# Optimization experiments

Hardware: AMD Instinct MI355X
Metric: run time of the kernel (lower is better)

## Reference

```python
import jax, jax.numpy as jnp
import numpy as np

NF = 64      # feature channels
DG = 8       # deformable groups
KH = 3       # kernel size
K = KH * KH  # kernel points
B, H, W = 2, 256, 256


def conv2d(x, w, b):
    # 3x3, stride 1, pad 1, NCHW
    y = jax.lax.conv_general_dilated(x, w, (1, 1), [(1, 1), (1, 1)],
                                     dimension_numbers=('NCHW', 'OIHW', 'NCHW'))
    return y + b[None, :, None, None]


def bilinear_gather(img, py, px):
    # img: [B,G,Cg,H,W]; py,px: [B,G,Kd,H,W] float pixel coords (zero padding outside)
    # returns [B,G,Cg,Kd,H,W]
    b, g, cg, h, w = img.shape
    kd = py.shape[2]
    y0 = jnp.floor(py)
    x0 = jnp.floor(px)
    wy = py - y0
    wx = px - x0
    imgf = img.reshape(b, g, cg, h * w)

    def tap(yi, xi, wt):
        valid = (yi >= 0) & (yi <= h - 1) & (xi >= 0) & (xi <= w - 1)
        idx = (jnp.clip(yi, 0, h - 1) * w + jnp.clip(xi, 0, w - 1)).astype(jnp.int32)
        idxf = idx.reshape(b, g, 1, kd * h * w)
        v = jnp.take_along_axis(imgf, jnp.broadcast_to(idxf, (b, g, cg, kd * h * w)), axis=-1)
        v = v.reshape(b, g, cg, kd, h, w)
        return v * (wt * valid)[:, :, None]

    return (tap(y0, x0, (1 - wy) * (1 - wx)) + tap(y0, x0 + 1, (1 - wy) * wx)
            + tap(y0 + 1, x0, wy * (1 - wx)) + tap(y0 + 1, x0 + 1, wy * wx))


def setup_inputs() -> dict:
    key = jax.random.key(0)
    ks = jax.random.split(key, 8)
    s = 0.05
    return {
        'nbr': jax.random.normal(ks[0], (B, NF, H, W), jnp.float32),
        'ref': jax.random.normal(ks[1], (B, NF, H, W), jnp.float32),
        'optical_flow': jax.random.normal(ks[2], (B, 2, H, W), jnp.float32),
        'conv1_w': jax.random.normal(ks[3], (NF, 2 * NF, KH, KH), jnp.float32) * s,
        'conv1_b': jnp.zeros((NF,), jnp.float32),
        'om_w': jax.random.normal(ks[4], (DG * 3 * K, NF + 2, KH, KH), jnp.float32) * s,
        'om_b': jnp.zeros((DG * 3 * K,), jnp.float32),
        'dcn_w': jax.random.normal(ks[5], (NF, NF, KH, KH), jnp.float32) * s,
        'dcn_b': jnp.zeros((NF,), jnp.float32),
    }


def reference(nbr, ref, optical_flow, conv1_w, conv1_b, om_w, om_b, dcn_w, dcn_b):
    b, c, h, w = nbr.shape
    dt = nbr.dtype
    gy, gx = jnp.meshgrid(jnp.arange(h, dtype=dt), jnp.arange(w, dtype=dt), indexing='ij')

    # ---- backwarp(nbr, flow): bilinear sample at (x+fx, y+fy), zero padding ----
    py = (gy[None] + optical_flow[:, 1])[:, None, None]  # [B,1,1,H,W]
    px = (gx[None] + optical_flow[:, 0])[:, None, None]
    nbr_warp = bilinear_gather(nbr[:, None], py, px).reshape(b, c, h, w)

    # ---- offset feature ----
    fea = jax.nn.relu(conv2d(jnp.concatenate([nbr_warp, ref], 1), conv1_w, conv1_b))

    # ---- FlowGuidedDCN offset/mask generation ----
    out = conv2d(jnp.concatenate([fea, optical_flow], 1), om_w, om_b)
    o1, o2, mask = jnp.split(out, 3, axis=1)
    offset = jnp.concatenate([o1, o2], 1)                       # [B, 2*DG*K, H, W]
    flow_rep = jnp.tile(optical_flow[:, ::-1], (1, offset.shape[1] // 2, 1, 1))
    offset = offset + flow_rep
    mask = jax.nn.sigmoid(mask)                                 # [B, DG*K, H, W]

    # ---- deformable conv v2 (stride 1, pad 1, dil 1) ----
    off = offset.reshape(b, DG, K, 2, h, w)
    dy, dx = off[:, :, :, 0], off[:, :, :, 1]                   # [B,DG,K,H,W]
    ky, kx = jnp.meshgrid(jnp.arange(KH, dtype=dt), jnp.arange(KH, dtype=dt), indexing='ij')
    base_y = gy[None] - 1 + ky.reshape(-1)[:, None, None]       # [K,H,W]
    base_x = gx[None] - 1 + kx.reshape(-1)[:, None, None]
    spy = base_y[None, None] + dy
    spx = base_x[None, None] + dx

    cg = c // DG
    sampled = bilinear_gather(nbr.reshape(b, DG, cg, h, w), spy, spx)  # [B,DG,Cg,K,H,W]
    m = mask.reshape(b, DG, 1, K, h, w)
    wr = dcn_w.reshape(dcn_w.shape[0], DG, cg, K)
    y = jnp.einsum('bgckhw,ogck->bohw', sampled * m, wr) + dcn_b[None, :, None, None]
    return y
```

## Files before the change

### kernel.cpp

```cpp
#include <hip/hip_runtime.h>
#include <math.h>

#define HW 65536
#define WD 256
#define HT 256

typedef short short8 __attribute__((ext_vector_type(8)));
typedef float f32x4 __attribute__((ext_vector_type(4)));
typedef __bf16 bf16x8 __attribute__((ext_vector_type(8)));

__device__ __forceinline__ short f2bf(float f) {
    union { float f; unsigned u; } v; v.f = f;
    unsigned r = (v.u + 0x7fffu + ((v.u >> 16) & 1u)) >> 16;
    return (short)r;
}

__device__ __forceinline__ float bf2f(short s) {
    union { unsigned u; float f; } v;
    v.u = ((unsigned)(unsigned short)s) << 16;
    return v.f;
}

__device__ __forceinline__ int iclamp(int v, int lo, int hi) {
    return v < lo ? lo : (v > hi ? hi : v);
}

struct Taps {
    int i00, i01, i10, i11;
    float w00, w01, w10, w11;
};

__device__ __forceinline__ Taps make_taps(float py, float px) {
    float fy0 = floorf(py), fx0 = floorf(px);
    float wy = py - fy0, wx = px - fx0;
    int y0 = (int)fy0, x0 = (int)fx0;
    int y1 = y0 + 1, x1 = x0 + 1;
    float vy0 = (y0 >= 0 && y0 <= HT - 1) ? 1.f : 0.f;
    float vy1 = (y1 >= 0 && y1 <= HT - 1) ? 1.f : 0.f;
    float vx0 = (x0 >= 0 && x0 <= WD - 1) ? 1.f : 0.f;
    float vx1 = (x1 >= 0 && x1 <= WD - 1) ? 1.f : 0.f;
    int yc0 = iclamp(y0, 0, HT - 1), yc1 = iclamp(y1, 0, HT - 1);
    int xc0 = iclamp(x0, 0, WD - 1), xc1 = iclamp(x1, 0, WD - 1);
    Taps t;
    t.i00 = yc0 * WD + xc0; t.i01 = yc0 * WD + xc1;
    t.i10 = yc1 * WD + xc0; t.i11 = yc1 * WD + xc1;
    t.w00 = (1.f - wy) * (1.f - wx) * vy0 * vx0;
    t.w01 = (1.f - wy) * wx * vy0 * vx1;
    t.w10 = wy * (1.f - wx) * vy1 * vx0;
    t.w11 = wy * wx * vy1 * vx1;
    return t;
}

__global__ __launch_bounds__(256) void pack_x1_kernel(
    const float* __restrict__ nbr, const float* __restrict__ ref,
    const float* __restrict__ flow, short* __restrict__ X1)
{
    __shared__ short tile[64 * 130];
    int blk = blockIdx.x;
    int b = blk >> 10;
    int grp = blk & 1023;
    int px = threadIdx.x & 63;
    int qq = threadIdx.x >> 6;
    int pos = grp * 64 + px;
    int yy = pos >> 8, xx = pos & 255;

    float fx = flow[b * 2 * HW + pos];
    float fy = flow[b * 2 * HW + HW + pos];
    Taps tp = make_taps((float)yy + fy, (float)xx + fx);

    const float* nb = nbr + (size_t)b * 64 * HW;
    const float* rf = ref + (size_t)b * 64 * HW;
    #pragma unroll
    for (int j = 0; j < 16; ++j) {
        int c = qq * 16 + j;
        const float* pc = nb + c * HW;
        float v = tp.w00 * pc[tp.i00] + tp.w01 * pc[tp.i01] +
                  tp.w10 * pc[tp.i10] + tp.w11 * pc[tp.i11];
        tile[px * 130 + c] = f2bf(v);
        tile[px * 130 + 64 + c] = f2bf(rf[c * HW + pos]);
    }
    __syncthreads();

    short* xo = X1 + ((size_t)b * HW + grp * 64) * 128;
    #pragma unroll
    for (int f8 = threadIdx.x; f8 < 1024; f8 += 256) {
        int p = (f8 * 8) >> 7;
        int c = (f8 * 8) & 127;
        short8 v;
        #pragma unroll
        for (int j = 0; j < 8; ++j) v[j] = tile[p * 130 + c + j];
        *(short8*)(xo + f8 * 8) = v;
    }
}

__global__ __launch_bounds__(256) void pack_nbr_kernel(
    const float* __restrict__ nbr, short* __restrict__ N2)
{
    __shared__ short tile[64 * 66];
    int blk = blockIdx.x;
    int b = blk >> 10;
    int grp = blk & 1023;
    int px = threadIdx.x & 63;
    int qq = threadIdx.x >> 6;
    int pos = grp * 64 + px;

    const float* nb = nbr + (size_t)b * 64 * HW;
    #pragma unroll
    for (int j = 0; j < 16; ++j) {
        int c = qq * 16 + j;
        tile[px * 66 + c] = f2bf(nb[c * HW + pos]);
    }
    __syncthreads();

    short* xo = N2 + (size_t)b * HW * 64;
    #pragma unroll
    for (int f8 = threadIdx.x; f8 < 512; f8 += 256) {
        int g = f8 >> 6;
        int p = f8 & 63;
        short8 v;
        #pragma unroll
        for (int j = 0; j < 8; ++j) v[j] = tile[p * 66 + g * 8 + j];
        *(short8*)(xo + ((size_t)g * HW + grp * 64 + p) * 8) = v;
    }
}

__global__ __launch_bounds__(256) void repack_w1_kernel(
    const float* __restrict__ w, short* __restrict__ wr)
{
    int t = blockIdx.x * 256 + threadIdx.x;
    int j = t & 7, q = (t >> 3) & 3, l = (t >> 5) & 15;
    int nt = (t >> 9) & 3, kc = t >> 11;
    int k = kc * 32 + q * 8 + j;
    int rs = k >> 7, c = k & 127;
    int n = nt * 16 + l;
    wr[t] = f2bf(w[(n * 128 + c) * 9 + rs]);
}

__global__ __launch_bounds__(256) void repack_w2_kernel(
    const float* __restrict__ w, short* __restrict__ wr)
{
    int t = blockIdx.x * 256 + threadIdx.x;
    if (t >= 155648) return;
    int j = t & 7, q = (t >> 3) & 3, l = (t >> 5) & 15;
    int nt = (t >> 9) & 15, kc = t >> 13;
    int n = nt * 16 + l;
    float v = 0.f;
    if (kc < 18) {
        int k = kc * 32 + q * 8 + j;
        int rs = k >> 6, c = k & 63;
        if (n < 216) v = w[(n * 66 + c) * 9 + rs];
    } else {
        int k18 = q * 8 + j;
        if (k18 < 18 && n < 216) {
            int tap = k18 >> 1, u = k18 & 1;
            v = w[(n * 66 + 64 + u) * 9 + tap];
        }
    }
    wr[t] = f2bf(v);
}

__global__ __launch_bounds__(256) void repack_dcn_kernel(
    const float* __restrict__ w, short* __restrict__ wr)
{
    int t = blockIdx.x * 256 + threadIdx.x;
    int j = t & 7, q = (t >> 3) & 3, l = (t >> 5) & 15;
    int rem = t >> 9;
    int nt = rem & 3;
    int gkc = rem >> 2;
    int kc = gkc % 3, g = gkc / 3;
    int Kidx = kc * 32 + q * 8 + j;
    int k = Kidx >> 3, c = Kidx & 7;
    int och = nt * 16 + l;
    float v = (k < 9) ? w[(och * 64 + g * 8 + c) * 9 + k] : 0.f;
    wr[t] = f2bf(v);
}

#define PADC1 128
__global__ __launch_bounds__(256) void conv1_mfma_kernel(
    const short* __restrict__ X1, const float* __restrict__ bias,
    const short* __restrict__ wr, short* __restrict__ X2)
{
    __shared__ short lds[198 * PADC1];
    const int tid = threadIdx.x;
    const int w = __builtin_amdgcn_readfirstlane(tid >> 6);
    const int l15 = tid & 15;
    const int q = (tid >> 4) & 3;
    const int blk = ((blockIdx.x & 7) << 8) | (blockIdx.x >> 3);
    const int xseg = blk & 3;
    const int yy = (blk >> 2) & 255;
    const int b = blk >> 10;
    const int x0 = xseg * 64;

    const short* xin = X1 + (size_t)b * HW * 128;
    for (int i = tid; i < 198 * 16; i += 256) {
        int c16 = i & 15;
        int pix = i >> 4;
        int r = pix / 66, xx = pix % 66;
        int gy = yy + r - 1, gx = x0 + xx - 1;
        short8 v = {0, 0, 0, 0, 0, 0, 0, 0};
        if (gy >= 0 && gy < HT && gx >= 0 && gx < WD)
            v = *(const short8*)(xin + ((size_t)((gy << 8) + gx)) * 128 + c16 * 8);
        *(short8*)(&lds[pix * PADC1 + (c16 ^ (pix & 7)) * 8]) = v;
    }
    __syncthreads();

    f32x4 acc[4] = {{0,0,0,0},{0,0,0,0},{0,0,0,0},{0,0,0,0}};
    const int bbase = l15 * 4 + q;

    #define LOADB1(kc_) (*(const short8*)(wr + ((size_t)(((kc_) * 4 + w) * 64 + bbase)) * 8))
    #define COMP1(kc_, bf_) { \
        int rs_ = (kc_) >> 2, cc_ = (kc_) & 3; \
        int r_ = rs_ / 3, s_ = rs_ % 3; \
        int rowb_ = r_ * 66 + s_ + l15; \
        _Pragma("unroll") \
        for (int mt = 0; mt < 4; ++mt) { \
            int row_ = rowb_ + mt * 16; \
            int col16_ = (cc_ * 4 + q) ^ (row_ & 7); \
            short8 a_ = *(const short8*)(&lds[row_ * PADC1 + col16_ * 8]); \
            acc[mt] = __builtin_amdgcn_mfma_f32_16x16x32_bf16(a_, bf_, acc[mt], 0, 0, 0); \
        } }

    short8 bA = LOADB1(0), bB;
    #pragma unroll 1
    for (int jj = 0; jj < 18; ++jj) {
        int kc0 = 2 * jj;
        bB = LOADB1(kc0 + 1);
        COMP1(kc0, bA);
        int kc2 = kc0 + 2; if (kc2 > 35) kc2 = 35;
        bA = LOADB1(kc2);
        COMP1(kc0 + 1, bB);
    }
    #undef LOADB1
    #undef COMP1

    float bv = bias[w * 16 + l15];
    short* xo = X2 + (size_t)b * HW * 64;
    #pragma unroll
    for (int mt = 0; mt < 4; ++mt) {
        #pragma unroll
        for (int rg = 0; rg < 4; ++rg) {
            int px = x0 + mt * 16 + q * 4 + rg;
            float v = fmaxf(acc[mt][rg] + bv, 0.f);
            xo[((size_t)((yy << 8) + px)) * 64 + w * 16 + l15] = f2bf(v);
        }
    }
}

#define PADX 64
__global__ __launch_bounds__(256) void om_mfma_kernel(
    const short* __restrict__ X2, const float* __restrict__ flow,
    const short* __restrict__ wr, const float* __restrict__ bias,
    float* __restrict__ omraw)
{
    __shared__ __align__(16) char ldsraw[30464];
    short* ldsA = (short*)ldsraw;
    short* A18  = (short*)(ldsraw + 25344);
    float* ldsT = (float*)ldsraw;

    const int tid = threadIdx.x;
    const int w = __builtin_amdgcn_readfirstlane(tid >> 6);
    const int l15 = tid & 15;
    const int q = (tid >> 4) & 3;
    const int blk = ((blockIdx.x & 7) << 8) | (blockIdx.x >> 3);
    const int xseg = blk & 3;
    const int yy = (blk >> 2) & 255;
    const int b = blk >> 10;
    const int x0 = xseg * 64;

    const short* xin = X2 + (size_t)b * HW * 64;
    for (int i = tid; i < 198 * 8; i += 256) {
        int c8 = i & 7;
        int pix = i >> 3;
        int r = pix / 66, xx = pix % 66;
        int gy = yy + r - 1, gx = x0 + xx - 1;
        short8 v = {0, 0, 0, 0, 0, 0, 0, 0};
        if (gy >= 0 && gy < HT && gx >= 0 && gx < WD)
            v = *(const short8*)(xin + ((size_t)((gy << 8) + gx)) * 64 + c8 * 8);
        *(short8*)(&ldsA[pix * PADX + (c8 ^ (pix & 7)) * 8]) = v;
    }
    for (int i = tid; i < 64 * 40; i += 256) {
        int p = i / 40, kk = i - p * 40;
        short v = 0;
        if (kk < 18) {
            int tap = kk >> 1, u = kk & 1;
            int gy = yy + tap / 3 - 1, gx = x0 + p + tap % 3 - 1;
            if (gy >= 0 && gy < HT && gx >= 0 && gx < WD)
                v = f2bf(flow[(size_t)(b * 2 + u) * HW + (gy << 8) + gx]);
        }
        A18[p * 40 + kk] = v;
    }
    __syncthreads();

    f32x4 acc[4][4];
    #pragma unroll
    for (int i = 0; i < 4; ++i)
        #pragma unroll
        for (int mt = 0; mt < 4; ++mt) acc[i][mt] = (f32x4){0,0,0,0};

    const int bbase = l15 * 4 + q;

    #define LOADB2(dst_, kc_) { \
        _Pragma("unroll") \
        for (int i = 0; i < 4; ++i) \
            dst_[i] = *(const short8*)(wr + ((size_t)(((kc_) * 16 + w * 4 + i) * 64 + bbase)) * 8); }
    #define COMP2(kc_, bf_) { \
        int rs_ = (kc_) >> 1, half_ = (kc_) & 1; \
        int r_ = rs_ / 3, s_ = rs_ % 3; \
        int rowb_ = r_ * 66 + s_ + l15; \
        short8 a_[4]; \
        _Pragma("unroll") \
        for (int mt = 0; mt < 4; ++mt) { \
            int row_ = rowb_ + mt * 16; \
            int col16_ = (half_ * 4 + q) ^ (row_ & 7); \
            a_[mt] = *(const short8*)(&ldsA[row_ * PADX + col16_ * 8]); \
        } \
        _Pragma("unroll") \
        for (int i = 0; i < 4; ++i) \
            _Pragma("unroll") \
            for (int mt = 0; mt < 4; ++mt) \
                acc[i][mt] = __builtin_amdgcn_mfma_f32_16x16x32_bf16(a_[mt], bf_[i], acc[i][mt], 0, 0, 0); }

    short8 bA[4], bB[4];
    LOADB2(bA, 0);
    #pragma unroll 1
    for (int jj = 0; jj < 9; ++jj) {
        int kc0 = 2 * jj;
        LOADB2(bB, kc0 + 1);
        COMP2(kc0, bA);
        LOADB2(bA, kc0 + 2);
        COMP2(kc0 + 1, bB);
    }
    #pragma unroll
    for (int mt = 0; mt < 4; ++mt) {
        short8 a_ = *(const short8*)(&A18[(mt * 16 + l15) * 40 + q * 8]);
        #pragma unroll
        for (int i = 0; i < 4; ++i)
            acc[i][mt] = __builtin_amdgcn_mfma_f32_16x16x32_bf16(a_, bA[i], acc[i][mt], 0, 0, 0);
    }
    #undef LOADB2
    #undef COMP2

    const int LT = 65;
    #pragma unroll 1
    for (int pass = 0; pass < 4; ++pass) {
        __syncthreads();
        if (w == pass) {
            #pragma unroll
            for (int i = 0; i < 4; ++i) {
                int chl = i * 16 + l15;
                #pragma unroll
                for (int mt = 0; mt < 4; ++mt)
                    #pragma unroll
                    for (int rg = 0; rg < 4; ++rg)
                        ldsT[chl * LT + mt * 16 + q * 4 + rg] = acc[i][mt][rg];
            }
        }
        __syncthreads();
        int chbase = pass * 64;
        for (int f = tid; f < 64 * 64; f += 256) {
            int chl = f >> 6, px = f & 63;
            int ch = chbase + chl;
            if (ch < 216) {
                float v = ldsT[chl * LT + px] + bias[ch];
                omraw[((size_t)b * 216 + ch) * HW + (yy << 8) + x0 + px] = v;
            }
        }
    }
}

__global__ __launch_bounds__(256) void dcn_mfma_kernel(
    const float* __restrict__ raw,
    const float* __restrict__ flow,
    const short* __restrict__ N2,
    const short* __restrict__ wrd,
    const float* __restrict__ bias,
    float* __restrict__ out)
{
    __shared__ __align__(16) char ldsraw[26624];
    short* bufA = (short*)ldsraw;
    short* bufB = (short*)(ldsraw + 13312);
    float* ldsT = (float*)ldsraw;

    const int tid = threadIdx.x;
    const int w = __builtin_amdgcn_readfirstlane(tid >> 6);
    const int l15 = tid & 15;
    const int q = (tid >> 4) & 3;
    const int qq = tid >> 6;
    const int px = tid & 63;

    const int blk = ((blockIdx.x & 7) << 8) | (blockIdx.x >> 3);
    const int b = blk >> 10;
    const int grp = blk & 1023;
    const int pos0 = grp * 64;
    const int pos = pos0 + px;
    const int yy = pos >> 8, xx = pos & 255;

    const float* rawb = raw + (size_t)b * 216 * HW + pos;
    const float fx = flow[b * 2 * HW + pos];
    const float fy = flow[b * 2 * HW + HW + pos];
    const short* n2b = N2 + (size_t)b * HW * 64;

    {
        short8 z = {0, 0, 0, 0, 0, 0, 0, 0};
        #pragma unroll
        for (int it = 0; it < 3; ++it) {
            int k = qq + 4 * it;
            if (k >= 9) {
                *(short8*)(&bufA[px * 104 + k * 8]) = z;
                *(short8*)(&bufB[px * 104 + k * 8]) = z;
            }
        }
    }

    f32x4 acc[4] = {{0,0,0,0},{0,0,0,0},{0,0,0,0},{0,0,0,0}};

    float rdy[3], rdx[3], rm[3];
    #pragma unroll
    for (int it = 0; it < 3; ++it) {
        int k = qq + 4 * it;
        rdy[it] = 0.f; rdx[it] = 0.f; rm[it] = 0.f;
        if (k < 9) {
            rdy[it] = rawb[(size_t)(2 * k) * HW];
            rdx[it] = rawb[(size_t)(2 * k + 1) * HW];
            rm[it]  = rawb[(size_t)(144 + k) * HW];
        }
    }

    {
        const short* nbg = n2b;
        float w00[3], w01[3], w10[3], w11[3];
        short8 a00[3], a01[3], a10[3], a11[3];
        #pragma unroll
        for (int it = 0; it < 3; ++it) {
            int k = qq + 4 * it;
            if (k < 9) {
                float dy = rdy[it] + fy, dx = rdx[it] + fx;
                float m = 1.f / (1.f + __expf(-rm[it]));
                Taps tp = make_taps((float)(yy - 1 + k / 3) + dy,
                                    (float)(xx - 1 + k % 3) + dx);
                w00[it] = tp.w00 * m; w01[it] = tp.w01 * m;
                w10[it] = tp.w10 * m; w11[it] = tp.w11 * m;
                a00[it] = *(const short8*)(nbg + (size_t)tp.i00 * 8);
                a01[it] = *(const short8*)(nbg + (size_t)tp.i01 * 8);
                a10[it] = *(const short8*)(nbg + (size_t)tp.i10 * 8);
                a11[it] = *(const short8*)(nbg + (size_t)tp.i11 * 8);
            }
        }
        #pragma unroll
        for (int it = 0; it < 3; ++it) {
            int k = qq + 4 * it;
            if (k < 9) {
                rdy[it] = rawb[(size_t)(18 + 2 * k) * HW];
                rdx[it] = rawb[(size_t)(18 + 2 * k + 1) * HW];
                rm[it]  = rawb[(size_t)(144 + 9 + k) * HW];
            }
        }
        #pragma unroll
        for (int it = 0; it < 3; ++it) {
            int k = qq + 4 * it;
            if (k < 9) {
                union { bf16x8 bv; short8 s; } u;
                #pragma unroll
                for (int c = 0; c < 8; ++c) {
                    float s = w00[it] * bf2f(a00[it][c]) + w01[it] * bf2f(a01[it][c]) +
                              w10[it] * bf2f(a10[it][c]) + w11[it] * bf2f(a11[it][c]);
                    u.bv[c] = (__bf16)s;
                }
                *(short8*)(&bufA[px * 104 + k * 8]) = u.s;
            }
        }
    }
    __syncthreads();

    #pragma unroll 1
    for (int g = 0; g < 8; ++g) {
        short* cur = (g & 1) ? bufB : bufA;
        short* nxt = (g & 1) ? bufA : bufB;

        float w00[3], w01[3], w10[3], w11[3];
        short8 a00[3], a01[3], a10[3], a11[3];
        if (g < 7) {
            const short* nbg = n2b + (size_t)(g + 1) * HW * 8;
            #pragma unroll
            for (int it = 0; it < 3; ++it) {
                int k = qq + 4 * it;
                if (k < 9) {
                    float dy = rdy[it] + fy, dx = rdx[it] + fx;
                    float m = 1.f / (1.f + __expf(-rm[it]));
                    Taps tp = make_taps((float)(yy - 1 + k / 3) + dy,
                                        (float)(xx - 1 + k % 3) + dx);
                    w00[it] = tp.w00 * m; w01[it] = tp.w01 * m;
                    w10[it] = tp.w10 * m; w11[it] = tp.w11 * m;
                    a00[it] = *(const short8*)(nbg + (size_t)tp.i00 * 8);
                    a01[it] = *(const short8*)(nbg + (size_t)tp.i01 * 8);
                    a10[it] = *(const short8*)(nbg + (size_t)tp.i10 * 8);
                    a11[it] = *(const short8*)(nbg + (size_t)tp.i11 * 8);
                }
            }
            if (g < 6) {
                #pragma unroll
                for (int it = 0; it < 3; ++it) {
                    int k = qq + 4 * it;
                    if (k < 9) {
                        rdy[it] = rawb[(size_t)((g + 2) * 18 + 2 * k) * HW];
                        rdx[it] = rawb[(size_t)((g + 2) * 18 + 2 * k + 1) * HW];
                        rm[it]  = rawb[(size_t)(144 + (g + 2) * 9 + k) * HW];
                    }
                }
            }
        }

        #pragma unroll
        for (int kc = 0; kc < 3; ++kc) {
            short8 bfrag = *(const short8*)(wrd +
                ((size_t)(((g * 3 + kc) * 4 + w) * 64 + l15 * 4 + q)) * 8);
            #pragma unroll
            for (int mt = 0; mt < 4; ++mt) {
                short8 a = *(const short8*)(&cur[(mt * 16 + l15) * 104 + kc * 32 + q * 8]);
                acc[mt] = __builtin_amdgcn_mfma_f32_16x16x32_bf16(a, bfrag, acc[mt], 0, 0, 0);
            }
        }

        if (g < 7) {
            #pragma unroll
            for (int it = 0; it < 3; ++it) {
                int k = qq + 4 * it;
                if (k < 9) {
                    union { bf16x8 bv; short8 s; } u;
                    #pragma unroll
                    for (int c = 0; c < 8; ++c) {
                        float s = w00[it] * bf2f(a00[it][c]) + w01[it] * bf2f(a01[it][c]) +
                                  w10[it] * bf2f(a10[it][c]) + w11[it] * bf2f(a11[it][c]);
                        u.bv[c] = (__bf16)s;
                    }
                    *(short8*)(&nxt[px * 104 + k * 8]) = u.s;
                }
            }
        }
        __syncthreads();
    }

    #pragma unroll
    for (int mt = 0; mt < 4; ++mt)
        #pragma unroll
        for (int rg = 0; rg < 4; ++rg)
            ldsT[(w * 16 + l15) * 65 + mt * 16 + q * 4 + rg] = acc[mt][rg];
    __syncthreads();
    float* ob = out + (size_t)b * 64 * HW + pos0;
    for (int f = tid; f < 4096; f += 256) {
        int och = f >> 6, p2 = f & 63;
        ob[(size_t)och * HW + p2] = ldsT[och * 65 + p2] + bias[och];
    }
}

extern "C" void kernel_launch(void* const* d_in, const int* in_sizes, int n_in,
                              void* d_out, int out_size, void* d_ws, size_t ws_size,
                              hipStream_t stream)
{
    const float* nbr  = (const float*)d_in[0];
    const float* ref  = (const float*)d_in[1];
    const float* flow = (const float*)d_in[2];
    const float* c1w  = (const float*)d_in[3];
    const float* c1b  = (const float*)d_in[4];
    const float* omw  = (const float*)d_in[5];
    const float* omb  = (const float*)d_in[6];
    const float* dw   = (const float*)d_in[7];
    const float* db   = (const float*)d_in[8];
    float* out = (float*)d_out;

    char* wsb = (char*)d_ws;
    short* X1    = (short*)(wsb);
    short* X2    = (short*)(wsb + 33554432);
    float* omraw = (float*)(wsb + 58720256);
    short* wr1   = (short*)(wsb + 171966464);
    short* wr2   = (short*)(wsb + 172113920);
    short* wrd   = (short*)(wsb + 172556288);
    short* N2    = X1;

    repack_w1_kernel<<<288, 256, 0, stream>>>(c1w, wr1);
    repack_w2_kernel<<<608, 256, 0, stream>>>(omw, wr2);
    repack_dcn_kernel<<<192, 256, 0, stream>>>(dw, wrd);
    pack_x1_kernel<<<2048, 256, 0, stream>>>(nbr, ref, flow, X1);
    conv1_mfma_kernel<<<2048, 256, 0, stream>>>(X1, c1b, wr1, X2);
    pack_nbr_kernel<<<2048, 256, 0, stream>>>(nbr, N2);
    om_mfma_kernel<<<2048, 256, 0, stream>>>(X2, flow, wr2, omb, omraw);
    dcn_mfma_kernel<<<2048, 256, 0, stream>>>(omraw, flow, N2, wrd, db, out);
}
```

Before: 361.8 us.

## Widen offset/mask conv tile to 128 pixels and vectorize output stores

The offset/mask convolution kernel now processes 128-pixel row segments per block instead of 64. Each weight fragment loaded from global memory therefore feeds twice as many MFMAs, and the launch uses half as many blocks. The epilogue writes float4 vectors with bias added, replacing scalar stores, and runs two transpose passes instead of four. In exchange the kernel needs 66 KB of LDS and twice the accumulator registers, which lowers occupancy. Launch bounds are set to 2 blocks per SM.

```diff
diff --git a/kernel.cpp b/kernel.cpp
--- a/kernel.cpp
+++ b/kernel.cpp
@@ -246,40 +246,43 @@
     }
 }
 
-#define PADX 64
-__global__ __launch_bounds__(256) void om_mfma_kernel(
+#define PADX2 64
+__global__ __launch_bounds__(256, 2) void om_mfma_kernel(
     const short* __restrict__ X2, const float* __restrict__ flow,
     const short* __restrict__ wr, const float* __restrict__ bias,
     float* __restrict__ omraw)
 {
-    __shared__ __align__(16) char ldsraw[30464];
+    __shared__ __align__(16) char ldsraw[67584];
     short* ldsA = (short*)ldsraw;
-    short* A18  = (short*)(ldsraw + 25344);
+    short* A18  = (short*)(ldsraw + 49920);
     float* ldsT = (float*)ldsraw;
 
     const int tid = threadIdx.x;
     const int w = __builtin_amdgcn_readfirstlane(tid >> 6);
     const int l15 = tid & 15;
     const int q = (tid >> 4) & 3;
-    const int blk = ((blockIdx.x & 7) << 8) | (blockIdx.x >> 3);
-    const int xseg = blk & 3;
-    const int yy = (blk >> 2) & 255;
-    const int b = blk >> 10;
-    const int x0 = xseg * 64;
+    const int blk = ((blockIdx.x & 7) << 7) | (blockIdx.x >> 3);
+    const int xseg = blk & 1;
+    const int yy = (blk >> 1) & 255;
+    const int b = blk >> 9;
+    const int x0 = xseg * 128;
 
     const short* xin = X2 + (size_t)b * HW * 64;
-    for (int i = tid; i < 198 * 8; i += 256) {
-        int c8 = i & 7;
-        int pix = i >> 3;
-        int r = pix / 66, xx = pix % 66;
-        int gy = yy + r - 1, gx = x0 + xx - 1;
-        short8 v = {0, 0, 0, 0, 0, 0, 0, 0};
-        if (gy >= 0 && gy < HT && gx >= 0 && gx < WD)
-            v = *(const short8*)(xin + ((size_t)((gy << 8) + gx)) * 64 + c8 * 8);
-        *(short8*)(&ldsA[pix * PADX + (c8 ^ (pix & 7)) * 8]) = v;
-    }
-    for (int i = tid; i < 64 * 40; i += 256) {
-        int p = i / 40, kk = i - p * 40;
+    #pragma unroll
+    for (int r = 0; r < 3; ++r) {
+        int gy = yy + r - 1;
+        for (int i = tid; i < 130 * 8; i += 256) {
+            int xx = i >> 3, c8 = i & 7;
+            int gx = x0 + xx - 1;
+            short8 v = {0, 0, 0, 0, 0, 0, 0, 0};
+            if (gy >= 0 && gy < HT && gx >= 0 && gx < WD)
+                v = *(const short8*)(xin + ((size_t)((gy << 8) + gx)) * 64 + c8 * 8);
+            int pix = r * 130 + xx;
+            *(short8*)(&ldsA[pix * PADX2 + (c8 ^ (pix & 7)) * 8]) = v;
+        }
+    }
+    for (int i = tid; i < 128 * 32; i += 256) {
+        int p = i >> 5, kk = i & 31;
         short v = 0;
         if (kk < 18) {
             int tap = kk >> 1, u = kk & 1;
@@ -287,15 +290,15 @@
             if (gy >= 0 && gy < HT && gx >= 0 && gx < WD)
                 v = f2bf(flow[(size_t)(b * 2 + u) * HW + (gy << 8) + gx]);
         }
-        A18[p * 40 + kk] = v;
+        A18[p * 34 + kk] = v;
     }
     __syncthreads();
 
-    f32x4 acc[4][4];
+    f32x4 acc[4][8];
     #pragma unroll
     for (int i = 0; i < 4; ++i)
         #pragma unroll
-        for (int mt = 0; mt < 4; ++mt) acc[i][mt] = (f32x4){0,0,0,0};
+        for (int mt = 0; mt < 8; ++mt) acc[i][mt] = (f32x4){0, 0, 0, 0};
 
     const int bbase = l15 * 4 + q;
 
@@ -306,19 +309,16 @@
     #define COMP2(kc_, bf_) { \
         int rs_ = (kc_) >> 1, half_ = (kc_) & 1; \
         int r_ = rs_ / 3, s_ = rs_ % 3; \
-        int rowb_ = r_ * 66 + s_ + l15; \
-        short8 a_[4]; \
+        int rowb_ = r_ * 130 + s_ + l15; \
         _Pragma("unroll") \
-        for (int mt = 0; mt < 4; ++mt) { \
+        for (int mt = 0; mt < 8; ++mt) { \
             int row_ = rowb_ + mt * 16; \
             int col16_ = (half_ * 4 + q) ^ (row_ & 7); \
-            a_[mt] = *(const short8*)(&ldsA[row_ * PADX + col16_ * 8]); \
-        } \
-        _Pragma("unroll") \
-        for (int i = 0; i < 4; ++i) \
+            short8 a_ = *(const short8*)(&ldsA[row_ * PADX2 + col16_ * 8]); \
             _Pragma("unroll") \
-            for (int mt = 0; mt < 4; ++mt) \
-                acc[i][mt] = __builtin_amdgcn_mfma_f32_16x16x32_bf16(a_[mt], bf_[i], acc[i][mt], 0, 0, 0); }
+            for (int i = 0; i < 4; ++i) \
+                acc[i][mt] = __builtin_amdgcn_mfma_f32_16x16x32_bf16(a_, bf_[i], acc[i][mt], 0, 0, 0); \
+        } }
 
     short8 bA[4], bB[4];
     LOADB2(bA, 0);
@@ -331,8 +331,8 @@
         COMP2(kc0 + 1, bB);
     }
     #pragma unroll
-    for (int mt = 0; mt < 4; ++mt) {
-        short8 a_ = *(const short8*)(&A18[(mt * 16 + l15) * 40 + q * 8]);
+    for (int mt = 0; mt < 8; ++mt) {
+        short8 a_ = *(const short8*)(&A18[(mt * 16 + l15) * 34 + q * 8]);
         #pragma unroll
         for (int i = 0; i < 4; ++i)
             acc[i][mt] = __builtin_amdgcn_mfma_f32_16x16x32_bf16(a_, bA[i], acc[i][mt], 0, 0, 0);
@@ -340,29 +340,30 @@
     #undef LOADB2
     #undef COMP2
 
-    const int LT = 65;
     #pragma unroll 1
-    for (int pass = 0; pass < 4; ++pass) {
+    for (int pass = 0; pass < 2; ++pass) {
         __syncthreads();
-        if (w == pass) {
+        if ((w >> 1) == pass) {
+            int ochl_base = (w & 1) * 64;
             #pragma unroll
             for (int i = 0; i < 4; ++i) {
-                int chl = i * 16 + l15;
+                int ochl = ochl_base + i * 16 + l15;
                 #pragma unroll
-                for (int mt = 0; mt < 4; ++mt)
+                for (int mt = 0; mt < 8; ++mt)
                     #pragma unroll
                     for (int rg = 0; rg < 4; ++rg)
-                        ldsT[chl * LT + mt * 16 + q * 4 + rg] = acc[i][mt][rg];
+                        ldsT[ochl * 132 + mt * 16 + q * 4 + rg] = acc[i][mt][rg];
             }
         }
         __syncthreads();
-        int chbase = pass * 64;
-        for (int f = tid; f < 64 * 64; f += 256) {
-            int chl = f >> 6, px = f & 63;
-            int ch = chbase + chl;
+        for (int f = tid; f < 128 * 32; f += 256) {
+            int chl = f >> 5, p16 = (f & 31) * 4;
+            int ch = pass * 128 + chl;
             if (ch < 216) {
-                float v = ldsT[chl * LT + px] + bias[ch];
-                omraw[((size_t)b * 216 + ch) * HW + (yy << 8) + x0 + px] = v;
+                f32x4 v = *(const f32x4*)(&ldsT[chl * 132 + p16]);
+                float bv = bias[ch];
+                v[0] += bv; v[1] += bv; v[2] += bv; v[3] += bv;
+                *(f32x4*)(&omraw[((size_t)b * 216 + ch) * HW + (yy << 8) + x0 + p16]) = v;
             }
         }
     }
@@ -583,6 +584,6 @@
     pack_x1_kernel<<<2048, 256, 0, stream>>>(nbr, ref, flow, X1);
     conv1_mfma_kernel<<<2048, 256, 0, stream>>>(X1, c1b, wr1, X2);
     pack_nbr_kernel<<<2048, 256, 0, stream>>>(nbr, N2);
-    om_mfma_kernel<<<2048, 256, 0, stream>>>(X2, flow, wr2, omb, omraw);
+    om_mfma_kernel<<<1024, 256, 0, stream>>>(X2, flow, wr2, omb, omraw);
     dcn_mfma_kernel<<<2048, 256, 0, stream>>>(omraw, flow, N2, wrd, db, out);
 }
```

After: 322.1 us. 1.12x faster.
